# Kernel optimization log

Hardware: AMD Instinct MI355X
Metric: run time of the kernel (lower is better)

Reference implementation:

```python
import jax, jax.numpy as jnp
import numpy as np

DIM, HEADS, DIM_HEAD = 256, 8, 32  # dim == heads * dim_head
EPS = 1e-5


def setup_inputs() -> dict:
    key = jax.random.key(0)
    ks = jax.random.split(key, 6)
    B, C, H, W = 16, DIM, 64, 64
    x = jax.random.normal(ks[0], (B, C, H, W), dtype=jnp.float32)
    # 1x1 conv weights stored as [out_ch, in_ch]
    w_qkv = jax.random.normal(ks[1], (3 * DIM, DIM), dtype=jnp.float32) * (1.0 / np.sqrt(DIM))
    w_out = jax.random.normal(ks[2], (DIM, DIM), dtype=jnp.float32) * (1.0 / np.sqrt(DIM))
    b_out = jax.random.normal(ks[3], (DIM,), dtype=jnp.float32) * 0.01
    ln_gamma = jnp.ones((DIM,), dtype=jnp.float32)
    ln_beta = jnp.zeros((DIM,), dtype=jnp.float32)
    return {"x": x, "w_qkv": w_qkv, "w_out": w_out, "b_out": b_out,
            "ln_gamma": ln_gamma, "ln_beta": ln_beta}


def _linear_attention(x, w_qkv, w_out, b_out, ln_gamma, ln_beta):
    B, C, H, W = x.shape
    d = C // HEADS
    # 1x1 conv == channel matmul
    qkv = jnp.einsum('bchw,oc->bohw', x, w_qkv)  # [B, 3C, H, W]
    q, k, v = jnp.split(qkv, 3, axis=1)
    # 'b (h d) x y -> b h x y d'
    def split_heads(t):
        t = t.reshape(B, HEADS, d, H, W)
        return t.transpose(0, 1, 3, 4, 2)  # b h x y d
    q, k, v = split_heads(q), split_heads(k), split_heads(v)
    q = jax.nn.softmax(q, axis=-1)   # over d (channel) dim
    k = jax.nn.softmax(k, axis=-2)   # over y spatial axis (faithful to torch dim=-2)
    context = jnp.einsum('bhxyd,bhxye->bhde', k, v)          # [B,H,d,d]
    out = jnp.einsum('bhde,bhxye->bhxyd', context, q)        # [B,H,X,Y,d]
    # 'b h x y d -> b (h d) x y'
    out = out.transpose(0, 1, 4, 2, 3).reshape(B, C, H, W)
    # output 1x1 conv + bias
    out = jnp.einsum('bchw,oc->bohw', out, w_out) + b_out[None, :, None, None]
    # LayerNorm over channel dim (permute to NHWC, norm last axis, permute back)
    y = out.transpose(0, 2, 3, 1)  # b h w c
    mu = jnp.mean(y, axis=-1, keepdims=True)
    var = jnp.var(y, axis=-1, keepdims=True)
    y = (y - mu) / jnp.sqrt(var + EPS) * ln_gamma + ln_beta
    return y.transpose(0, 3, 1, 2)


def reference(x, w_qkv, w_out, b_out, ln_gamma, ln_beta):
    return _linear_attention(x, w_qkv, w_out, b_out, ln_gamma, ln_beta)
```

## Files before the change

kernel.cpp:

```cpp
#include <hip/hip_runtime.h>
#include <hip/hip_bf16.h>

#define NB 16
#define CDIM 256
#define NHEADS 8
#define DH 32
#define NSP 4096
#define O3 768

typedef __bf16 bf16;
typedef bf16 bf16x4 __attribute__((ext_vector_type(4)));
typedef bf16 bf16x8 __attribute__((ext_vector_type(8)));
typedef float f32x4 __attribute__((ext_vector_type(4)));
typedef float f32x16 __attribute__((ext_vector_type(16)));

static __device__ __forceinline__ float bf2f(bf16 x){ return (float)x; }
static __device__ __forceinline__ bf16 f2bf(float x){ return (bf16)x; }

static __device__ __forceinline__ void gld16(const bf16* g, bf16* l){
    __builtin_amdgcn_global_load_lds((const __attribute__((address_space(1))) void*)g,
                                     (__attribute__((address_space(3))) void*)l, 16, 0, 0);
}

__global__ void k_transpose(const float* __restrict__ x, bf16* __restrict__ xT){
    __shared__ bf16 tile[64][72];
    int b = blockIdx.z;
    int c0 = blockIdx.y * 64;
    int n0 = blockIdx.x * 64;
    int t = threadIdx.x;
    const float* xb = x + (size_t)b * CDIM * NSP;
    #pragma unroll
    for (int i = 0; i < 4; ++i){
        int lin = i*256 + t;
        int c = lin >> 4;
        int n4 = (lin & 15) * 4;
        f32x4 f = *(const f32x4*)(xb + (size_t)(c0 + c)*NSP + n0 + n4);
        bf16x4 v4;
        #pragma unroll
        for (int j = 0; j < 4; ++j) v4[j] = f2bf(f[j]);
        *(bf16x4*)&tile[c][n4] = v4;
    }
    __syncthreads();
    bf16* xTb = xT + (size_t)b * NSP * CDIM;
    #pragma unroll
    for (int i = 0; i < 2; ++i){
        int lin = i*256 + t;
        int n = lin >> 3;
        int c8 = (lin & 7) * 8;
        bf16x8 v;
        #pragma unroll
        for (int j = 0; j < 8; ++j) v[j] = tile[c8+j][n];
        *(bf16x8*)(xTb + (size_t)(n0+n)*CDIM + c0 + c8) = v;
    }
}

__global__ void k_wcvt(const float* __restrict__ w, bf16* __restrict__ w2){
    int idx = (blockIdx.x*256 + threadIdx.x) * 4;
    f32x4 f = *(const f32x4*)(w + idx);
    bf16x4 v;
    #pragma unroll
    for (int j=0;j<4;j++) v[j] = f2bf(f[j]);
    *(bf16x4*)(w2 + idx) = v;
}

__global__ __launch_bounds__(256) void k_qkv(const bf16* __restrict__ w2,
                                             const bf16* __restrict__ xT,
                                             bf16* __restrict__ qT,
                                             bf16* __restrict__ kv){
    __shared__ union {
        bf16 Bs[32768];
        bf16 ep[128*136];
    } sm;
    int bid = blockIdx.x;
    int xcd = bid & 7, slot = bid >> 3;
    int m  = slot % 6;
    int ntile = xcd*64 + slot/6;
    int b  = ntile >> 5;
    int n0 = (ntile & 31) * 128;
    int m0 = m * 128;
    int t = threadIdx.x;
    int wv = t >> 6, lane = t & 63;

    #pragma unroll
    for (int j=0;j<16;j++){
        int base_r = wv*32 + j*2;
        int r = base_r + (lane>>5);
        int c = (lane & 31) ^ (r & 7);
        const bf16* g = xT + ((size_t)b*NSP + n0 + r)*CDIM + c*8;
        gld16(g, &sm.Bs[(size_t)base_r*256]);
    }
    __syncthreads();

    int brow[8], brx[8];
    #pragma unroll
    for (int ni=0;ni<8;ni++){
        int r = ni*16 + (lane&15);
        brow[ni] = r*32; brx[ni] = r & 7;
    }
    int arow = m0 + wv*32 + (lane&15);
    int acol = (lane>>4)*8;

    f32x4 acc[2][8];
    #pragma unroll
    for (int i=0;i<16;i++) ((f32x4*)acc)[i] = (f32x4){0.f,0.f,0.f,0.f};

    bf16x8 af0 = *(const bf16x8*)(w2 + (size_t)(arow     )*CDIM + acol);
    bf16x8 af1 = *(const bf16x8*)(w2 + (size_t)(arow + 16)*CDIM + acol);
    #pragma unroll
    for (int k0=0;k0<8;k0++){
        bf16x8 an0, an1;
        if (k0 < 7){
            an0 = *(const bf16x8*)(w2 + (size_t)(arow     )*CDIM + (k0+1)*32 + acol);
            an1 = *(const bf16x8*)(w2 + (size_t)(arow + 16)*CDIM + (k0+1)*32 + acol);
        }
        int cbase = (lane>>4) + k0*4;
        bf16x8 bfr[8];
        #pragma unroll
        for (int ni=0;ni<8;ni++)
            bfr[ni] = *(const bf16x8*)&sm.Bs[(size_t)(brow[ni] + (cbase ^ brx[ni]))*8];
        #pragma unroll
        for (int ni=0;ni<8;ni++)
            acc[0][ni] = __builtin_amdgcn_mfma_f32_16x16x32_bf16(af0, bfr[ni], acc[0][ni], 0, 0, 0);
        #pragma unroll
        for (int ni=0;ni<8;ni++)
            acc[1][ni] = __builtin_amdgcn_mfma_f32_16x16x32_bf16(af1, bfr[ni], acc[1][ni], 0, 0, 0);
        af0 = an0; af1 = an1;
    }
    __syncthreads();

    if (m0 < 256){
        #pragma unroll
        for (int ni=0;ni<8;ni++){
            float mx = -1e30f;
            #pragma unroll
            for (int mi=0;mi<2;mi++)
                #pragma unroll
                for (int r=0;r<4;r++) mx = fmaxf(mx, acc[mi][ni][r]);
            mx = fmaxf(mx, __shfl_xor(mx, 16, 64));
            mx = fmaxf(mx, __shfl_xor(mx, 32, 64));
            float s = 0.f;
            #pragma unroll
            for (int mi=0;mi<2;mi++)
                #pragma unroll
                for (int r=0;r<4;r++){
                    float e = __expf(acc[mi][ni][r] - mx);
                    acc[mi][ni][r] = e; s += e;
                }
            s += __shfl_xor(s, 16, 64);
            s += __shfl_xor(s, 32, 64);
            float inv = 1.f/s;
            #pragma unroll
            for (int mi=0;mi<2;mi++)
                #pragma unroll
                for (int r=0;r<4;r++) acc[mi][ni][r] *= inv;
        }
        #pragma unroll
        for (int mi=0;mi<2;mi++)
            #pragma unroll
            for (int ni=0;ni<8;ni++){
                int n_loc = ni*16 + (lane&15);
                int o_loc = wv*32 + mi*16 + (lane>>4)*4;
                bf16x4 v4;
                #pragma unroll
                for (int r=0;r<4;r++) v4[r] = f2bf(acc[mi][ni][r]);
                *(bf16x4*)&sm.ep[n_loc*136 + o_loc] = v4;
            }
        __syncthreads();
        bf16* qTb = qT + (size_t)b * NSP * CDIM;
        #pragma unroll
        for (int p=0;p<8;p++){
            int task = p*256 + t;
            int n_loc = task >> 4, seg = task & 15;
            bf16x8 v = *(const bf16x8*)&sm.ep[n_loc*136 + seg*8];
            *(bf16x8*)(qTb + (size_t)(n0+n_loc)*CDIM + m0 + seg*8) = v;
        }
    } else {
        if (m0 < 512){
            #pragma unroll
            for (int mi=0;mi<2;mi++)
                #pragma unroll
                for (int r=0;r<4;r++)
                    #pragma unroll
                    for (int grp=0;grp<2;grp++){
                        float mx = -1e30f;
                        #pragma unroll
                        for (int q=0;q<4;q++) mx = fmaxf(mx, acc[mi][grp*4+q][r]);
                        #pragma unroll
                        for (int msk=1; msk<16; msk<<=1) mx = fmaxf(mx, __shfl_xor(mx, msk, 64));
                        float s = 0.f;
                        #pragma unroll
                        for (int q=0;q<4;q++){
                            float e = __expf(acc[mi][grp*4+q][r] - mx);
                            acc[mi][grp*4+q][r] = e; s += e;
                        }
                        #pragma unroll
                        for (int msk=1; msk<16; msk<<=1) s += __shfl_xor(s, msk, 64);
                        float inv = 1.f/s;
                        #pragma unroll
                        for (int q=0;q<4;q++) acc[mi][grp*4+q][r] *= inv;
                    }
        }
        #pragma unroll
        for (int mi=0;mi<2;mi++)
            #pragma unroll
            for (int ni=0;ni<8;ni++){
                int n_loc = ni*16 + (lane&15);
                int c_loc = wv*32 + mi*16 + (lane>>4)*4;
                #pragma unroll
                for (int r=0;r<4;r++) sm.ep[(c_loc+r)*136 + n_loc] = f2bf(acc[mi][ni][r]);
            }
        __syncthreads();
        bf16* kvb = kv + (size_t)b * 512 * NSP;
        int c0t = m0 - 256;
        #pragma unroll
        for (int p=0;p<8;p++){
            int task = p*256 + t;
            int c_loc = task >> 4, seg = task & 15;
            bf16x8 v = *(const bf16x8*)&sm.ep[c_loc*136 + seg*8];
            *(bf16x8*)(kvb + (size_t)(c0t+c_loc)*NSP + n0 + seg*8) = v;
        }
    }
}

__global__ __launch_bounds__(256) void k_context(const bf16* __restrict__ kv,
                                                 float* __restrict__ ctx_p){
    int blk = blockIdx.x;
    int bh = blk >> 2;
    int chunk = blk & 3;
    int b = bh >> 3, h = bh & 7;
    int wave = threadIdx.x >> 6, lane = threadIdx.x & 63;
    int nbase = chunk*1024 + wave*256;
    int row = lane & 31;
    int koff = (lane >> 5) * 8;
    const bf16* kp = kv + ((size_t)b*512 +       h*DH + row)*NSP + nbase + koff;
    const bf16* vp = kv + ((size_t)b*512 + 256 + h*DH + row)*NSP + nbase + koff;
    f32x16 acc;
    #pragma unroll
    for (int i=0;i<16;i++) acc[i] = 0.f;
    #pragma unroll
    for (int s=0; s<16; s++){
        bf16x8 a  = *(const bf16x8*)(kp + s*16);
        bf16x8 bb = *(const bf16x8*)(vp + s*16);
        acc = __builtin_amdgcn_mfma_f32_32x32x16_bf16(a, bb, acc, 0, 0, 0);
    }
    float* dst = ctx_p + ((size_t)bh*16 + chunk*4 + wave)*1024;
    #pragma unroll
    for (int r=0;r<16;r++){
        int d = (r&3) + 8*(r>>2) + 4*(lane>>5);
        dst[d*32 + (lane&31)] = acc[r];
    }
}

__global__ void k_merge(const float* __restrict__ w_out, const float* __restrict__ ctx_p,
                        bf16* __restrict__ W2){
    __shared__ float ctxs[32][32];
    int bh = blockIdx.x;
    int b = bh >> 3, h = bh & 7;
    int t = threadIdx.x;
    const float* base = ctx_p + (size_t)bh*16*1024;
    #pragma unroll
    for (int i=0;i<4;i++){
        int idx = i*256 + t;
        float s = 0.f;
        #pragma unroll
        for (int p=0;p<16;p++) s += base[p*1024 + idx];
        ((float*)ctxs)[idx] = s;
    }
    __syncthreads();
    int o = t;
    const float* wrow = w_out + (size_t)o*CDIM + h*DH;
    float wv[32];
    #pragma unroll
    for (int d=0;d<32;d++) wv[d] = wrow[d];
    bf16* dst = W2 + ((size_t)b*CDIM + o)*CDIM + h*DH;
    #pragma unroll
    for (int g=0;g<4;g++){
        bf16x8 o8;
        #pragma unroll
        for (int jj=0;jj<8;jj++){
            int e = g*8 + jj;
            float s = 0.f;
            #pragma unroll
            for (int d=0;d<32;d++) s += wv[d]*ctxs[d][e];
            o8[jj] = f2bf(s);
        }
        *(bf16x8*)(dst + g*8) = o8;
    }
}

__global__ __launch_bounds__(256) void k_out_ln(const bf16* __restrict__ W2,
                                                const bf16* __restrict__ qT,
                                                const float* __restrict__ bout,
                                                const float* __restrict__ gamma,
                                                const float* __restrict__ beta,
                                                float* __restrict__ out){
    __shared__ union {
        bf16 Bs[16384];
        float Y[256*66];
    } sm;
    __shared__ float red[2][4][64];
    __shared__ float mu_s[64], rstd_s[64];
    int bid = blockIdx.x;
    int xcd = bid & 7, slot = bid >> 3;
    int b  = slot >> 3;
    int n0 = (xcd*8 + (slot & 7)) * 64;
    int t = threadIdx.x, wv = t>>6, lane = t&63;

    const bf16* qTb = qT + (size_t)b * NSP * CDIM;
    #pragma unroll
    for (int j=0;j<8;j++){
        int base_r = wv*16 + j*2;
        int r = base_r + (lane>>5);
        int c = (lane & 31) ^ (r & 7);
        gld16(qTb + (size_t)(n0 + r)*CDIM + c*8, &sm.Bs[(size_t)base_r*256]);
    }
    __syncthreads();

    int brow[4], brx[4];
    #pragma unroll
    for (int ni=0;ni<4;ni++){
        int r = ni*16 + (lane&15);
        brow[ni] = r*32; brx[ni] = r & 7;
    }
    const bf16* Ab = W2 + (size_t)b*CDIM*CDIM;
    int arow = wv*64 + (lane&15);
    int acol = (lane>>4)*8;

    f32x4 acc[4][4];
    #pragma unroll
    for (int i=0;i<16;i++) ((f32x4*)acc)[i] = (f32x4){0.f,0.f,0.f,0.f};

    bf16x8 af[4], an[4];
    #pragma unroll
    for (int mi=0;mi<4;mi++)
        af[mi] = *(const bf16x8*)(Ab + (size_t)(arow + mi*16)*CDIM + acol);
    #pragma unroll 2
    for (int k0=0;k0<8;k0++){
        if (k0 < 7){
            #pragma unroll
            for (int mi=0;mi<4;mi++)
                an[mi] = *(const bf16x8*)(Ab + (size_t)(arow + mi*16)*CDIM + (k0+1)*32 + acol);
        }
        int cbase = (lane>>4) + k0*4;
        bf16x8 bfr[4];
        #pragma unroll
        for (int ni=0;ni<4;ni++)
            bfr[ni] = *(const bf16x8*)&sm.Bs[(size_t)(brow[ni] + (cbase ^ brx[ni]))*8];
        #pragma unroll
        for (int mi=0;mi<4;mi++)
            #pragma unroll
            for (int ni=0;ni<4;ni++)
                acc[mi][ni] = __builtin_amdgcn_mfma_f32_16x16x32_bf16(af[mi], bfr[ni], acc[mi][ni], 0, 0, 0);
        #pragma unroll
        for (int mi=0;mi<4;mi++) af[mi] = an[mi];
    }
    __syncthreads();
    #pragma unroll
    for (int mi=0;mi<4;mi++)
        #pragma unroll
        for (int ni=0;ni<4;ni++)
            #pragma unroll
            for (int r=0;r<4;r++){
                int o = wv*64 + mi*16 + (lane>>4)*4 + r;
                int n = ni*16 + (lane&15);
                sm.Y[o*66 + n] = acc[mi][ni][r];
            }
    __syncthreads();
    int n = t & 63, q = t >> 6;
    float s = 0.f, s2 = 0.f;
    for (int o=64*q; o<64*q+64; o++){
        float y = sm.Y[o*66+n] + bout[o];
        s += y; s2 += y*y;
    }
    red[0][q][n] = s; red[1][q][n] = s2;
    __syncthreads();
    if (t < 64){
        float S  = red[0][0][t]+red[0][1][t]+red[0][2][t]+red[0][3][t];
        float S2 = red[1][0][t]+red[1][1][t]+red[1][2][t]+red[1][3][t];
        float mu = S * (1.f/256.f);
        float var = S2*(1.f/256.f) - mu*mu;
        mu_s[t] = mu; rstd_s[t] = rsqrtf(var + 1e-5f);
    }
    __syncthreads();
    float mu = mu_s[n], rstd = rstd_s[n];
    size_t ob = (size_t)b*CDIM*NSP + n0 + n;
    for (int o=64*q; o<64*q+64; o++){
        float y = sm.Y[o*66+n] + bout[o];
        out[ob + (size_t)o*NSP] = (y - mu)*rstd*gamma[o] + beta[o];
    }
}

extern "C" void kernel_launch(void* const* d_in, const int* in_sizes, int n_in,
                              void* d_out, int out_size, void* d_ws, size_t ws_size,
                              hipStream_t stream){
    const float* x     = (const float*)d_in[0];
    const float* w_qkv = (const float*)d_in[1];
    const float* w_out = (const float*)d_in[2];
    const float* b_out = (const float*)d_in[3];
    const float* gamma = (const float*)d_in[4];
    const float* beta  = (const float*)d_in[5];
    float* out = (float*)d_out;
    char* ws = (char*)d_ws;
    bf16*  xT    = (bf16*) ws;
    float* ctx_p = (float*)ws;
    bf16*  qT    = (bf16*)(ws + 33554432ull);
    bf16*  kv    = (bf16*)(ws + 67108864ull);
    bf16*  W2    = (bf16*)(ws + 134742016ull);
    bf16*  w2    = (bf16*)(ws + 136839168ull);

    k_wcvt     <<<dim3(192),       256, 0, stream>>>(w_qkv, w2);
    k_transpose<<<dim3(64, 4, NB), 256, 0, stream>>>(x, xT);
    k_qkv      <<<dim3(3072),      256, 0, stream>>>(w2, xT, qT, kv);
    k_context  <<<dim3(512),       256, 0, stream>>>(kv, ctx_p);
    k_merge    <<<dim3(128),       256, 0, stream>>>(w_out, ctx_p, W2);
    k_out_ln   <<<dim3(1024),      256, 0, stream>>>(W2, qT, b_out, gamma, beta, out);
}
```

Measured before the change: 248.5 us.

## Fuse K/V projection with context reduction and shrink output-LN tiles

The combined QKV GEMM is split in two. A new kernel computes the K and V projections for a 64-column tile, applies the K softmax, stages K and V in shared memory and immediately computes per-tile partial d×d context matrices, so the bf16 K/V tensor is never written to or read back from global memory. The merge kernel now reduces 64 partials per head instead of 16, and the output+LayerNorm kernel uses 32-column tiles with a higher occupancy hint. The cost is more partial-context traffic and a larger merge reduction, plus the Q projection now reloads xT separately.

```diff
diff --git a/kernel.cpp b/kernel.cpp
--- a/kernel.cpp
+++ b/kernel.cpp
@@ -63,18 +63,17 @@
     *(bf16x4*)(w2 + idx) = v;
 }
 
-__global__ __launch_bounds__(256) void k_qkv(const bf16* __restrict__ w2,
-                                             const bf16* __restrict__ xT,
-                                             bf16* __restrict__ qT,
-                                             bf16* __restrict__ kv){
+__global__ __launch_bounds__(256) void k_q(const bf16* __restrict__ w2,
+                                           const bf16* __restrict__ xT,
+                                           bf16* __restrict__ qT){
     __shared__ union {
         bf16 Bs[32768];
         bf16 ep[128*136];
     } sm;
     int bid = blockIdx.x;
     int xcd = bid & 7, slot = bid >> 3;
-    int m  = slot % 6;
-    int ntile = xcd*64 + slot/6;
+    int m  = slot & 1;
+    int ntile = xcd*64 + (slot >> 1);
     int b  = ntile >> 5;
     int n0 = (ntile & 31) * 128;
     int m0 = m * 128;
@@ -128,126 +127,179 @@
     }
     __syncthreads();
 
-    if (m0 < 256){
+    #pragma unroll
+    for (int ni=0;ni<8;ni++){
+        float mx = -1e30f;
+        #pragma unroll
+        for (int mi=0;mi<2;mi++)
+            #pragma unroll
+            for (int r=0;r<4;r++) mx = fmaxf(mx, acc[mi][ni][r]);
+        mx = fmaxf(mx, __shfl_xor(mx, 16, 64));
+        mx = fmaxf(mx, __shfl_xor(mx, 32, 64));
+        float s = 0.f;
+        #pragma unroll
+        for (int mi=0;mi<2;mi++)
+            #pragma unroll
+            for (int r=0;r<4;r++){
+                float e = __expf(acc[mi][ni][r] - mx);
+                acc[mi][ni][r] = e; s += e;
+            }
+        s += __shfl_xor(s, 16, 64);
+        s += __shfl_xor(s, 32, 64);
+        float inv = 1.f/s;
+        #pragma unroll
+        for (int mi=0;mi<2;mi++)
+            #pragma unroll
+            for (int r=0;r<4;r++) acc[mi][ni][r] *= inv;
+    }
+    #pragma unroll
+    for (int mi=0;mi<2;mi++)
         #pragma unroll
         for (int ni=0;ni<8;ni++){
-            float mx = -1e30f;
-            #pragma unroll
-            for (int mi=0;mi<2;mi++)
-                #pragma unroll
-                for (int r=0;r<4;r++) mx = fmaxf(mx, acc[mi][ni][r]);
-            mx = fmaxf(mx, __shfl_xor(mx, 16, 64));
-            mx = fmaxf(mx, __shfl_xor(mx, 32, 64));
-            float s = 0.f;
-            #pragma unroll
-            for (int mi=0;mi<2;mi++)
-                #pragma unroll
-                for (int r=0;r<4;r++){
+            int n_loc = ni*16 + (lane&15);
+            int o_loc = wv*32 + mi*16 + (lane>>4)*4;
+            bf16x4 v4;
+            #pragma unroll
+            for (int r=0;r<4;r++) v4[r] = f2bf(acc[mi][ni][r]);
+            *(bf16x4*)&sm.ep[n_loc*136 + o_loc] = v4;
+        }
+    __syncthreads();
+    bf16* qTb = qT + (size_t)b * NSP * CDIM;
+    #pragma unroll
+    for (int p=0;p<8;p++){
+        int task = p*256 + t;
+        int n_loc = task >> 4, seg = task & 15;
+        bf16x8 v = *(const bf16x8*)&sm.ep[n_loc*136 + seg*8];
+        *(bf16x8*)(qTb + (size_t)(n0+n_loc)*CDIM + m0 + seg*8) = v;
+    }
+}
+
+__global__ __launch_bounds__(1024,4) void k_kvctx(const bf16* __restrict__ w2,
+                                                  const bf16* __restrict__ xT,
+                                                  float* __restrict__ ctx_p){
+    __shared__ union {
+        bf16 Bs[16384];
+        bf16 cb[16384];
+    } sm;
+    int bid = blockIdx.x;
+    int xcd = bid & 7, slot = bid >> 3;
+    int g = xcd*128 + slot;
+    int b = g >> 6;
+    int ntloc = g & 63;
+    int n0 = ntloc * 64;
+    int t = threadIdx.x;
+    int wv = t >> 6, lane = t & 63;
+
+    #pragma unroll
+    for (int j=0;j<2;j++){
+        int base_r = wv*4 + j*2;
+        int r = base_r + (lane>>5);
+        int c = (lane & 31) ^ (r & 7);
+        gld16(xT + ((size_t)b*NSP + n0 + r)*CDIM + c*8, &sm.Bs[(size_t)base_r*256]);
+    }
+    __syncthreads();
+
+    int brow[4], brx[4];
+    #pragma unroll
+    for (int ni=0;ni<4;ni++){
+        int r = ni*16 + (lane&15);
+        brow[ni] = r*32; brx[ni] = r & 7;
+    }
+    int arow = 256 + wv*32 + (lane&15);
+    int acol = (lane>>4)*8;
+
+    f32x4 acc[2][4];
+    #pragma unroll
+    for (int i=0;i<8;i++) ((f32x4*)acc)[i] = (f32x4){0.f,0.f,0.f,0.f};
+
+    bf16x8 af0 = *(const bf16x8*)(w2 + (size_t)(arow     )*CDIM + acol);
+    bf16x8 af1 = *(const bf16x8*)(w2 + (size_t)(arow + 16)*CDIM + acol);
+    #pragma unroll
+    for (int k0=0;k0<8;k0++){
+        bf16x8 an0, an1;
+        if (k0 < 7){
+            an0 = *(const bf16x8*)(w2 + (size_t)(arow     )*CDIM + (k0+1)*32 + acol);
+            an1 = *(const bf16x8*)(w2 + (size_t)(arow + 16)*CDIM + (k0+1)*32 + acol);
+        }
+        int cbase = (lane>>4) + k0*4;
+        bf16x8 bfr[4];
+        #pragma unroll
+        for (int ni=0;ni<4;ni++)
+            bfr[ni] = *(const bf16x8*)&sm.Bs[(size_t)(brow[ni] + (cbase ^ brx[ni]))*8];
+        #pragma unroll
+        for (int ni=0;ni<4;ni++)
+            acc[0][ni] = __builtin_amdgcn_mfma_f32_16x16x32_bf16(af0, bfr[ni], acc[0][ni], 0, 0, 0);
+        #pragma unroll
+        for (int ni=0;ni<4;ni++)
+            acc[1][ni] = __builtin_amdgcn_mfma_f32_16x16x32_bf16(af1, bfr[ni], acc[1][ni], 0, 0, 0);
+        af0 = an0; af1 = an1;
+    }
+
+    if (wv < 8){
+        #pragma unroll
+        for (int mi=0;mi<2;mi++)
+            #pragma unroll
+            for (int r=0;r<4;r++){
+                float mx = -1e30f;
+                #pragma unroll
+                for (int ni=0;ni<4;ni++) mx = fmaxf(mx, acc[mi][ni][r]);
+                #pragma unroll
+                for (int msk=1; msk<16; msk<<=1) mx = fmaxf(mx, __shfl_xor(mx, msk, 64));
+                float s = 0.f;
+                #pragma unroll
+                for (int ni=0;ni<4;ni++){
                     float e = __expf(acc[mi][ni][r] - mx);
                     acc[mi][ni][r] = e; s += e;
                 }
-            s += __shfl_xor(s, 16, 64);
-            s += __shfl_xor(s, 32, 64);
-            float inv = 1.f/s;
+                #pragma unroll
+                for (int msk=1; msk<16; msk<<=1) s += __shfl_xor(s, msk, 64);
+                float inv = 1.f/s;
+                #pragma unroll
+                for (int ni=0;ni<4;ni++) acc[mi][ni][r] *= inv;
+            }
+    }
+
+    #pragma unroll
+    for (int ph=0; ph<2; ++ph){
+        __syncthreads();
+        int isv  = wv >> 3;
+        int wloc = wv & 7;
+        if ((wloc >> 2) == ph){
+            int base = isv * 8192;
+            int w03 = wloc & 3;
             #pragma unroll
             for (int mi=0;mi<2;mi++)
                 #pragma unroll
-                for (int r=0;r<4;r++) acc[mi][ni][r] *= inv;
-        }
-        #pragma unroll
-        for (int mi=0;mi<2;mi++)
-            #pragma unroll
-            for (int ni=0;ni<8;ni++){
-                int n_loc = ni*16 + (lane&15);
-                int o_loc = wv*32 + mi*16 + (lane>>4)*4;
-                bf16x4 v4;
-                #pragma unroll
-                for (int r=0;r<4;r++) v4[r] = f2bf(acc[mi][ni][r]);
-                *(bf16x4*)&sm.ep[n_loc*136 + o_loc] = v4;
+                for (int ni=0;ni<4;ni++)
+                    #pragma unroll
+                    for (int r=0;r<4;r++){
+                        int row = w03*32 + mi*16 + (lane>>4)*4 + r;
+                        int n = ni*16 + (lane&15);
+                        sm.cb[base + row*64 + (((n>>3) ^ (row&7))<<3) + (n&7)] = f2bf(acc[mi][ni][r]);
+                    }
+        }
+        __syncthreads();
+        if (wv < 4){
+            f32x16 cacc;
+            #pragma unroll
+            for (int i=0;i<16;i++) cacc[i] = 0.f;
+            int rr = wv*32 + (lane&31);
+            int swz = (rr & 7) << 3;
+            #pragma unroll
+            for (int s=0;s<4;s++){
+                int nseg = s*2 + (lane>>5);
+                int off = rr*64 + (((nseg<<3) ^ swz));
+                bf16x8 ka = *(const bf16x8*)&sm.cb[off];
+                bf16x8 vb = *(const bf16x8*)&sm.cb[8192 + off];
+                cacc = __builtin_amdgcn_mfma_f32_32x32x16_bf16(ka, vb, cacc, 0, 0, 0);
             }
-        __syncthreads();
-        bf16* qTb = qT + (size_t)b * NSP * CDIM;
-        #pragma unroll
-        for (int p=0;p<8;p++){
-            int task = p*256 + t;
-            int n_loc = task >> 4, seg = task & 15;
-            bf16x8 v = *(const bf16x8*)&sm.ep[n_loc*136 + seg*8];
-            *(bf16x8*)(qTb + (size_t)(n0+n_loc)*CDIM + m0 + seg*8) = v;
-        }
-    } else {
-        if (m0 < 512){
-            #pragma unroll
-            for (int mi=0;mi<2;mi++)
-                #pragma unroll
-                for (int r=0;r<4;r++)
-                    #pragma unroll
-                    for (int grp=0;grp<2;grp++){
-                        float mx = -1e30f;
-                        #pragma unroll
-                        for (int q=0;q<4;q++) mx = fmaxf(mx, acc[mi][grp*4+q][r]);
-                        #pragma unroll
-                        for (int msk=1; msk<16; msk<<=1) mx = fmaxf(mx, __shfl_xor(mx, msk, 64));
-                        float s = 0.f;
-                        #pragma unroll
-                        for (int q=0;q<4;q++){
-                            float e = __expf(acc[mi][grp*4+q][r] - mx);
-                            acc[mi][grp*4+q][r] = e; s += e;
-                        }
-                        #pragma unroll
-                        for (int msk=1; msk<16; msk<<=1) s += __shfl_xor(s, msk, 64);
-                        float inv = 1.f/s;
-                        #pragma unroll
-                        for (int q=0;q<4;q++) acc[mi][grp*4+q][r] *= inv;
-                    }
-        }
-        #pragma unroll
-        for (int mi=0;mi<2;mi++)
-            #pragma unroll
-            for (int ni=0;ni<8;ni++){
-                int n_loc = ni*16 + (lane&15);
-                int c_loc = wv*32 + mi*16 + (lane>>4)*4;
-                #pragma unroll
-                for (int r=0;r<4;r++) sm.ep[(c_loc+r)*136 + n_loc] = f2bf(acc[mi][ni][r]);
+            float* dst = ctx_p + ((size_t)(b*8 + ph*4 + wv)*64 + ntloc)*1024;
+            #pragma unroll
+            for (int r=0;r<16;r++){
+                int d = (r&3) + 8*(r>>2) + 4*(lane>>5);
+                dst[d*32 + (lane&31)] = cacc[r];
             }
-        __syncthreads();
-        bf16* kvb = kv + (size_t)b * 512 * NSP;
-        int c0t = m0 - 256;
-        #pragma unroll
-        for (int p=0;p<8;p++){
-            int task = p*256 + t;
-            int c_loc = task >> 4, seg = task & 15;
-            bf16x8 v = *(const bf16x8*)&sm.ep[c_loc*136 + seg*8];
-            *(bf16x8*)(kvb + (size_t)(c0t+c_loc)*NSP + n0 + seg*8) = v;
-        }
-    }
-}
-
-__global__ __launch_bounds__(256) void k_context(const bf16* __restrict__ kv,
-                                                 float* __restrict__ ctx_p){
-    int blk = blockIdx.x;
-    int bh = blk >> 2;
-    int chunk = blk & 3;
-    int b = bh >> 3, h = bh & 7;
-    int wave = threadIdx.x >> 6, lane = threadIdx.x & 63;
-    int nbase = chunk*1024 + wave*256;
-    int row = lane & 31;
-    int koff = (lane >> 5) * 8;
-    const bf16* kp = kv + ((size_t)b*512 +       h*DH + row)*NSP + nbase + koff;
-    const bf16* vp = kv + ((size_t)b*512 + 256 + h*DH + row)*NSP + nbase + koff;
-    f32x16 acc;
-    #pragma unroll
-    for (int i=0;i<16;i++) acc[i] = 0.f;
-    #pragma unroll
-    for (int s=0; s<16; s++){
-        bf16x8 a  = *(const bf16x8*)(kp + s*16);
-        bf16x8 bb = *(const bf16x8*)(vp + s*16);
-        acc = __builtin_amdgcn_mfma_f32_32x32x16_bf16(a, bb, acc, 0, 0, 0);
-    }
-    float* dst = ctx_p + ((size_t)bh*16 + chunk*4 + wave)*1024;
-    #pragma unroll
-    for (int r=0;r<16;r++){
-        int d = (r&3) + 8*(r>>2) + 4*(lane>>5);
-        dst[d*32 + (lane&31)] = acc[r];
+        }
     }
 }
 
@@ -257,13 +309,12 @@
     int bh = blockIdx.x;
     int b = bh >> 3, h = bh & 7;
     int t = threadIdx.x;
-    const float* base = ctx_p + (size_t)bh*16*1024;
+    const float* base = ctx_p + (size_t)bh*64*1024;
     #pragma unroll
     for (int i=0;i<4;i++){
         int idx = i*256 + t;
         float s = 0.f;
-        #pragma unroll
-        for (int p=0;p<16;p++) s += base[p*1024 + idx];
+        for (int p=0;p<64;p++) s += base[p*1024 + idx];
         ((float*)ctxs)[idx] = s;
     }
     __syncthreads();
@@ -288,37 +339,37 @@
     }
 }
 
-__global__ __launch_bounds__(256) void k_out_ln(const bf16* __restrict__ W2,
-                                                const bf16* __restrict__ qT,
-                                                const float* __restrict__ bout,
-                                                const float* __restrict__ gamma,
-                                                const float* __restrict__ beta,
-                                                float* __restrict__ out){
+__global__ __launch_bounds__(256,4) void k_out_ln(const bf16* __restrict__ W2,
+                                                  const bf16* __restrict__ qT,
+                                                  const float* __restrict__ bout,
+                                                  const float* __restrict__ gamma,
+                                                  const float* __restrict__ beta,
+                                                  float* __restrict__ out){
     __shared__ union {
-        bf16 Bs[16384];
-        float Y[256*66];
+        bf16 Bs[8192];
+        float Y[256*33];
     } sm;
-    __shared__ float red[2][4][64];
-    __shared__ float mu_s[64], rstd_s[64];
+    __shared__ float red[2][8][32];
+    __shared__ float mu_s[32], rstd_s[32];
     int bid = blockIdx.x;
     int xcd = bid & 7, slot = bid >> 3;
-    int b  = slot >> 3;
-    int n0 = (xcd*8 + (slot & 7)) * 64;
+    int b  = slot >> 4;
+    int n0 = (xcd*16 + (slot & 15)) * 32;
     int t = threadIdx.x, wv = t>>6, lane = t&63;
 
     const bf16* qTb = qT + (size_t)b * NSP * CDIM;
     #pragma unroll
-    for (int j=0;j<8;j++){
-        int base_r = wv*16 + j*2;
+    for (int j=0;j<4;j++){
+        int base_r = wv*8 + j*2;
         int r = base_r + (lane>>5);
         int c = (lane & 31) ^ (r & 7);
         gld16(qTb + (size_t)(n0 + r)*CDIM + c*8, &sm.Bs[(size_t)base_r*256]);
     }
     __syncthreads();
 
-    int brow[4], brx[4];
-    #pragma unroll
-    for (int ni=0;ni<4;ni++){
+    int brow[2], brx[2];
+    #pragma unroll
+    for (int ni=0;ni<2;ni++){
         int r = ni*16 + (lane&15);
         brow[ni] = r*32; brx[ni] = r & 7;
     }
@@ -326,15 +377,15 @@
     int arow = wv*64 + (lane&15);
     int acol = (lane>>4)*8;
 
-    f32x4 acc[4][4];
-    #pragma unroll
-    for (int i=0;i<16;i++) ((f32x4*)acc)[i] = (f32x4){0.f,0.f,0.f,0.f};
+    f32x4 acc[4][2];
+    #pragma unroll
+    for (int i=0;i<8;i++) ((f32x4*)acc)[i] = (f32x4){0.f,0.f,0.f,0.f};
 
     bf16x8 af[4], an[4];
     #pragma unroll
     for (int mi=0;mi<4;mi++)
         af[mi] = *(const bf16x8*)(Ab + (size_t)(arow + mi*16)*CDIM + acol);
-    #pragma unroll 2
+    #pragma unroll
     for (int k0=0;k0<8;k0++){
         if (k0 < 7){
             #pragma unroll
@@ -342,14 +393,14 @@
                 an[mi] = *(const bf16x8*)(Ab + (size_t)(arow + mi*16)*CDIM + (k0+1)*32 + acol);
         }
         int cbase = (lane>>4) + k0*4;
-        bf16x8 bfr[4];
-        #pragma unroll
-        for (int ni=0;ni<4;ni++)
+        bf16x8 bfr[2];
+        #pragma unroll
+        for (int ni=0;ni<2;ni++)
             bfr[ni] = *(const bf16x8*)&sm.Bs[(size_t)(brow[ni] + (cbase ^ brx[ni]))*8];
         #pragma unroll
         for (int mi=0;mi<4;mi++)
             #pragma unroll
-            for (int ni=0;ni<4;ni++)
+            for (int ni=0;ni<2;ni++)
                 acc[mi][ni] = __builtin_amdgcn_mfma_f32_16x16x32_bf16(af[mi], bfr[ni], acc[mi][ni], 0, 0, 0);
         #pragma unroll
         for (int mi=0;mi<4;mi++) af[mi] = an[mi];
@@ -358,25 +409,26 @@
     #pragma unroll
     for (int mi=0;mi<4;mi++)
         #pragma unroll
-        for (int ni=0;ni<4;ni++)
+        for (int ni=0;ni<2;ni++)
             #pragma unroll
             for (int r=0;r<4;r++){
                 int o = wv*64 + mi*16 + (lane>>4)*4 + r;
                 int n = ni*16 + (lane&15);
-                sm.Y[o*66 + n] = acc[mi][ni][r];
+                sm.Y[o*33 + n] = acc[mi][ni][r];
             }
     __syncthreads();
-    int n = t & 63, q = t >> 6;
+    int n = t & 31, q = t >> 5;
     float s = 0.f, s2 = 0.f;
-    for (int o=64*q; o<64*q+64; o++){
-        float y = sm.Y[o*66+n] + bout[o];
+    for (int o=32*q; o<32*q+32; o++){
+        float y = sm.Y[o*33+n] + bout[o];
         s += y; s2 += y*y;
     }
     red[0][q][n] = s; red[1][q][n] = s2;
     __syncthreads();
-    if (t < 64){
-        float S  = red[0][0][t]+red[0][1][t]+red[0][2][t]+red[0][3][t];
-        float S2 = red[1][0][t]+red[1][1][t]+red[1][2][t]+red[1][3][t];
+    if (t < 32){
+        float S = 0.f, S2 = 0.f;
+        #pragma unroll
+        for (int p=0;p<8;p++){ S += red[0][p][t]; S2 += red[1][p][t]; }
         float mu = S * (1.f/256.f);
         float var = S2*(1.f/256.f) - mu*mu;
         mu_s[t] = mu; rstd_s[t] = rsqrtf(var + 1e-5f);
@@ -384,8 +436,8 @@
     __syncthreads();
     float mu = mu_s[n], rstd = rstd_s[n];
     size_t ob = (size_t)b*CDIM*NSP + n0 + n;
-    for (int o=64*q; o<64*q+64; o++){
-        float y = sm.Y[o*66+n] + bout[o];
+    for (int o=32*q; o<32*q+32; o++){
+        float y = sm.Y[o*33+n] + bout[o];
         out[ob + (size_t)o*NSP] = (y - mu)*rstd*gamma[o] + beta[o];
     }
 }
@@ -402,16 +454,15 @@
     float* out = (float*)d_out;
     char* ws = (char*)d_ws;
     bf16*  xT    = (bf16*) ws;
-    float* ctx_p = (float*)ws;
     bf16*  qT    = (bf16*)(ws + 33554432ull);
-    bf16*  kv    = (bf16*)(ws + 67108864ull);
+    float* ctx_p = (float*)(ws + 67108864ull);
     bf16*  W2    = (bf16*)(ws + 134742016ull);
     bf16*  w2    = (bf16*)(ws + 136839168ull);
 
-    k_wcvt     <<<dim3(192),       256, 0, stream>>>(w_qkv, w2);
-    k_transpose<<<dim3(64, 4, NB), 256, 0, stream>>>(x, xT);
-    k_qkv      <<<dim3(3072),      256, 0, stream>>>(w2, xT, qT, kv);
-    k_context  <<<dim3(512),       256, 0, stream>>>(kv, ctx_p);
-    k_merge    <<<dim3(128),       256, 0, stream>>>(w_out, ctx_p, W2);
-    k_out_ln   <<<dim3(1024),      256, 0, stream>>>(W2, qT, b_out, gamma, beta, out);
-}
+    k_wcvt     <<<dim3(192),       256,  0, stream>>>(w_qkv, w2);
+    k_transpose<<<dim3(64, 4, NB), 256,  0, stream>>>(x, xT);
+    k_kvctx    <<<dim3(1024),      1024, 0, stream>>>(w2, xT, ctx_p);
+    k_q        <<<dim3(1024),      256,  0, stream>>>(w2, xT, qT);
+    k_merge    <<<dim3(128),       256,  0, stream>>>(w_out, ctx_p, W2);
+    k_out_ln   <<<dim3(2048),      256,  0, stream>>>(W2, qT, b_out, gamma, beta, out);
+}
```

Result: slower. 267.0 us (+7.4%).
